# Optimization experiments

Hardware: AMD Instinct MI355X
Metric: run time of the kernel (lower is better)

Reference implementation:

```python
import jax, jax.numpy as jnp
import numpy as np

B, S, E, H = 4, 1024, 1024, 16
HD = E // H  # 64


def setup_inputs() -> dict:
    key = jax.random.key(0)
    ks = jax.random.split(key, 9)
    scale = 1.0 / np.sqrt(E)
    x = jax.random.normal(ks[0], (B, S, E), dtype=jnp.float32)
    attention_mask = jnp.ones((B, S, S), dtype=jnp.int32)
    # per-head projection weights, batched over heads: [H, E, HD]
    Wq = jax.random.normal(ks[1], (H, E, HD), dtype=jnp.float32) * scale
    Wk = jax.random.normal(ks[2], (H, E, HD), dtype=jnp.float32) * scale
    Wv = jax.random.normal(ks[3], (H, E, HD), dtype=jnp.float32) * scale
    bq = jax.random.normal(ks[4], (H, HD), dtype=jnp.float32) * scale
    bk = jax.random.normal(ks[5], (H, HD), dtype=jnp.float32) * scale
    bv = jax.random.normal(ks[6], (H, HD), dtype=jnp.float32) * scale
    # output projection, torch Linear convention: [out_features, in_features]
    Wo = jax.random.normal(ks[7], (E, E), dtype=jnp.float32) * scale
    bo = jax.random.normal(ks[8], (E,), dtype=jnp.float32) * scale
    return {"x": x, "attention_mask": attention_mask, "Wq": Wq, "bq": bq,
            "Wk": Wk, "bk": bk, "Wv": Wv, "bv": bv, "Wo": Wo, "bo": bo}


def reference(x, attention_mask, Wq, bq, Wk, bk, Wv, bv, Wo, bo):
    # batched-over-heads QKV projections: (B,S,E) x (H,E,HD) -> (B,H,S,HD)
    q = jnp.einsum('bse,hed->bhsd', x, Wq) + bq[None, :, None, :]
    k = jnp.einsum('bse,hed->bhsd', x, Wk) + bk[None, :, None, :]
    v = jnp.einsum('bse,hed->bhsd', x, Wv) + bv[None, :, None, :]
    scores = jnp.einsum('bhsd,bhtd->bhst', q, k) / jnp.sqrt(jnp.float32(HD))
    mask = attention_mask[:, None, :, :]  # (B,1,S,S) broadcast over heads
    scores = jnp.where(mask == 0, -jnp.inf, scores)
    weights = jax.nn.softmax(scores, axis=-1)
    out = jnp.einsum('bhst,bhtd->bhsd', weights, v)
    # concat heads on last dim: (B,S,H*HD) == (B,S,E)
    out = out.transpose(0, 2, 1, 3).reshape(B, S, E)
    return out @ Wo.T + bo
```

## Files before the change

### kernel.cpp

```cpp
#include <hip/hip_runtime.h>
#include <hip/hip_bf16.h>

#define NB 4
#define SEQ 1024
#define EMB 1024
#define NH 16
#define HD 64

typedef unsigned short u16;
typedef __attribute__((ext_vector_type(8))) __bf16 bf16x8;
typedef __attribute__((ext_vector_type(8))) short short8;
typedef __attribute__((ext_vector_type(4))) float floatx4;

__device__ inline u16 f2b_rn(float f) {
    union { float f; unsigned int i; } x; x.f = f;
    unsigned int r = (x.i + 0x7FFFu + ((x.i >> 16) & 1u)) >> 16;
    return (u16)r;
}
__device__ inline bf16x8 s2b(short8 v) {
    union { short8 s; bf16x8 b; } x; x.s = v; return x.b;
}

__device__ inline void gload_lds16(const void* g, void* l) {
    __builtin_amdgcn_global_load_lds(
        (const __attribute__((address_space(1))) void*)g,
        (__attribute__((address_space(3))) void*)l, 16, 0, 0);
}

__device__ inline bf16x8 ldsfrag(const u16* base, int r, int c) {
    return s2b(*(const short8*)&base[r * 64 + (c ^ ((r & 7) * 8))]);
}

__device__ inline void cvt8(const float* __restrict__ s, u16* __restrict__ d) {
    float4 a = *(const float4*)(s);
    float4 b = *(const float4*)(s + 4);
    union { u16 u[8]; int4 v; } o;
    o.u[0] = f2b_rn(a.x); o.u[1] = f2b_rn(a.y); o.u[2] = f2b_rn(a.z); o.u[3] = f2b_rn(a.w);
    o.u[4] = f2b_rn(b.x); o.u[5] = f2b_rn(b.y); o.u[6] = f2b_rn(b.z); o.u[7] = f2b_rn(b.w);
    *(int4*)(d) = o.v;
}

__global__ __launch_bounds__(256) void prep(
    const float* __restrict__ x, const float* __restrict__ Wq,
    const float* __restrict__ Wk, const float* __restrict__ Wv,
    u16* __restrict__ xb, u16* __restrict__ Wt)
{
    __shared__ u16 T[64 * 80];
    int bx = blockIdx.x;
    int tid = threadIdx.x;

    if (bx < 512) {
        #pragma unroll
        for (int c = 0; c < 4; ++c) {
            int i = (bx * 4 + c) * 2048 + tid * 8;
            cvt8(x + i, xb + i);
        }
    } else {
        int bx2 = bx - 512;
        int e0 = (bx2 & 15) * 64;
        int ph = bx2 >> 4;
        int p = ph >> 4, h = ph & 15;
        const float* W = (p == 0 ? Wq : (p == 1 ? Wk : Wv)) + h * (EMB * HD);
        #pragma unroll
        for (int c = 0; c < 2; ++c) {
            int flat = c * 2048 + tid * 8;
            int r = flat >> 6;
            int d = flat & 63;
            cvt8(W + (size_t)(e0 + r) * HD + d, &T[r * 80 + d]);
        }
        __syncthreads();
        int d = tid >> 2;
        int ec = tid & 3;
        union { u16 u[16]; int4 v[2]; } tmp;
        #pragma unroll
        for (int i = 0; i < 16; ++i) tmp.u[i] = T[(ec * 16 + i) * 80 + d];
        u16* dst = Wt + ((size_t)(p * NH + h) * HD + d) * EMB + e0 + ec * 16;
        *(int4*)(dst) = tmp.v[0];
        *(int4*)(dst + 8) = tmp.v[1];
    }
}

__global__ __launch_bounds__(256) void qkv_gemm(
    const u16* __restrict__ x,
    const u16* __restrict__ Wt2,
    const float* __restrict__ bq, const float* __restrict__ bk, const float* __restrict__ bv,
    const float* __restrict__ Wo, const int* __restrict__ mask,
    u16* __restrict__ Q, u16* __restrict__ K, u16* __restrict__ Vt,
    u16* __restrict__ Wob, unsigned long long* __restrict__ bits)
{
    __shared__ u16 As[128 * 64];
    __shared__ u16 Bs[128 * 64];

    int gid = blockIdx.x;
    int tid = threadIdx.x;

    if (gid >= 768) {
        if (gid < 1280) {
            int i = (gid - 768) * 2048 + tid * 8;
            cvt8(Wo + i, Wob + i);
        } else {
            int base = (gid - 1280) * 16 + (tid >> 6) * 4;
            int lane = tid & 63;
            #pragma unroll
            for (int i = 0; i < 4; ++i) {
                int gw = base + i;
                int m = mask[(size_t)gw * 64 + lane];
                unsigned long long bl = __ballot(m != 0);
                if (lane == 0) bits[gw] = bl;
            }
        }
        return;
    }

    int n0 = (gid % 24) * 128;
    int m0 = (gid / 24) * 128;
    int w = tid >> 6, lane = tid & 63, quad = lane >> 4, ln = lane & 15;
    int wm = w & 1, wn = w >> 1;

    floatx4 acc[4][4] = {};

    for (int k0 = 0; k0 < EMB; k0 += 64) {
        __syncthreads();
        #pragma unroll
        for (int i = 0; i < 4; ++i) {
            int flat0 = i * 256 + (tid & 192);
            int flat = flat0 + lane;
            int r = flat >> 3;
            int c = ((flat & 7) ^ (r & 7)) * 8;
            gload_lds16(x   + (size_t)(m0 + r) * EMB + k0 + c, As + flat0 * 8);
            gload_lds16(Wt2 + (size_t)(n0 + r) * EMB + k0 + c, Bs + flat0 * 8);
        }
        __syncthreads();

        #pragma unroll
        for (int kk = 0; kk < 2; ++kk) {
            bf16x8 a[4], bf[4];
            #pragma unroll
            for (int mt = 0; mt < 4; ++mt)
                a[mt] = ldsfrag(As, wm * 64 + mt * 16 + ln, kk * 32 + quad * 8);
            #pragma unroll
            for (int nc = 0; nc < 4; ++nc)
                bf[nc] = ldsfrag(Bs, wn * 64 + nc * 16 + ln, kk * 32 + quad * 8);
            #pragma unroll
            for (int mt = 0; mt < 4; ++mt)
                #pragma unroll
                for (int nc = 0; nc < 4; ++nc)
                    acc[mt][nc] = __builtin_amdgcn_mfma_f32_16x16x32_bf16(a[mt], bf[nc], acc[mt][nc], 0, 0, 0);
        }
    }

    int p = n0 >> 10;
    const float* bias = (p == 0 ? bq : (p == 1 ? bk : bv));
    if (p < 2) {
        u16* Out = (p == 0) ? Q : K;
        float qs = (p == 0) ? 0.125f * 1.44269504f : 1.0f;
        #pragma unroll
        for (int nc = 0; nc < 4; ++nc) {
            int n = n0 + wn * 64 + nc * 16 + ln;
            int h = (n >> 6) & 15, d = n & 63;
            float bv_ = bias[n & 1023];
            #pragma unroll
            for (int mt = 0; mt < 4; ++mt) {
                #pragma unroll
                for (int reg = 0; reg < 4; ++reg) {
                    int m = m0 + wm * 64 + mt * 16 + quad * 4 + reg;
                    int b_ = m >> 10, s = m & 1023;
                    Out[((size_t)(b_ * NH + h) * SEQ + s) * HD + d] = f2b_rn((acc[mt][nc][reg] + bv_) * qs);
                }
            }
        }
    } else {
        #pragma unroll
        for (int nc = 0; nc < 4; ++nc) {
            int n = n0 + wn * 64 + nc * 16 + ln;
            int h = (n >> 6) & 15, d = n & 63;
            float bv_ = bias[n & 1023];
            #pragma unroll
            for (int mt = 0; mt < 4; ++mt) {
                int m = m0 + wm * 64 + mt * 16 + quad * 4;
                int b_ = m >> 10, s = m & 1023;
                union { u16 u[4]; uint2 v; } pk;
                #pragma unroll
                for (int reg = 0; reg < 4; ++reg)
                    pk.u[reg] = f2b_rn(acc[mt][nc][reg] + bv_);
                *(uint2*)&Vt[((size_t)(b_ * NH + h) * HD + d) * SEQ + s] = pk.v;
            }
        }
    }
}

__global__ __launch_bounds__(128) void attn(
    const u16* __restrict__ Q, const u16* __restrict__ K, const u16* __restrict__ Vt,
    const unsigned long long* __restrict__ bits,
    u16* __restrict__ Aout)
{
    const int PP = 72;
    __shared__ u16 Ks[64 * 64];
    __shared__ u16 Vs[80 * 64];
    __shared__ u16 Ps[64 * PP];

    int bh = blockIdx.x;
    int q0 = blockIdx.y * 64;
    int b = bh >> 4, h = bh & 15;
    const u16* Qb = Q  + (size_t)bh * SEQ * HD;
    const u16* Kb = K  + (size_t)bh * SEQ * HD;
    const u16* Vb = Vt + (size_t)bh * HD * SEQ;

    int tid = threadIdx.x;
    int w = tid >> 6, lane = tid & 63, quad = lane >> 4, ln = lane & 15;

    if (tid < 16) *(uint2*)&Vs[64 * 64 + tid * 4] = make_uint2(0x3F803F80u, 0x3F803F80u);

    bf16x8 qf[2][2];
    #pragma unroll
    for (int s = 0; s < 2; ++s) {
        const u16* qp = Qb + (size_t)(q0 + w * 32 + s * 16 + ln) * HD + quad * 8;
        union { int4 i; bf16x8 b; } c0, c1;
        c0.i = *(const int4*)(qp);
        c1.i = *(const int4*)(qp + 32);
        qf[s][0] = c0.b; qf[s][1] = c1.b;
    }

    floatx4 o[2][5] = {};

    for (int tt = 0; tt < SEQ / 64; ++tt) {
        int t0 = tt * 64;
        __syncthreads();
        #pragma unroll
        for (int i = 0; i < 4; ++i) {
            int flat0 = i * 128 + (tid & 64);
            int flat = flat0 + lane;
            int r = flat >> 3;
            int c = ((flat & 7) ^ (r & 7)) * 8;
            gload_lds16(Kb + (size_t)(t0 + r) * HD + c, Ks + flat0 * 8);
            gload_lds16(Vb + (size_t)r * SEQ + t0 + c, Vs + flat0 * 8);
        }
        __syncthreads();

        floatx4 sc[2][4] = {};
        #pragma unroll
        for (int kk = 0; kk < 2; ++kk) {
            bf16x8 kf[4];
            #pragma unroll
            for (int tb = 0; tb < 4; ++tb)
                kf[tb] = ldsfrag(Ks, tb * 16 + ln, kk * 32 + quad * 8);
            #pragma unroll
            for (int s = 0; s < 2; ++s)
                #pragma unroll
                for (int tb = 0; tb < 4; ++tb)
                    sc[s][tb] = __builtin_amdgcn_mfma_f32_16x16x32_bf16(kf[tb], qf[s][kk], sc[s][tb], 0, 0, 0);
        }

        #pragma unroll
        for (int s = 0; s < 2; ++s) {
            unsigned long long bm = bits[((size_t)b * SEQ + q0 + w * 32 + s * 16 + ln) * 16 + tt];
            if (__any(bm != ~0ull)) {
                #pragma unroll
                for (int tb = 0; tb < 4; ++tb)
                    #pragma unroll
                    for (int reg = 0; reg < 4; ++reg)
                        if (!((bm >> (tb * 16 + quad * 4 + reg)) & 1)) sc[s][tb][reg] = -1e30f;
            }
        }

        #pragma unroll
        for (int s = 0; s < 2; ++s) {
            int mrow = w * 32 + s * 16 + ln;
            #pragma unroll
            for (int tb = 0; tb < 4; ++tb) {
                union { float f; unsigned int i; } e0_, e1_, e2_, e3_;
                e0_.f = __builtin_amdgcn_exp2f(sc[s][tb][0]);
                e1_.f = __builtin_amdgcn_exp2f(sc[s][tb][1]);
                e2_.f = __builtin_amdgcn_exp2f(sc[s][tb][2]);
                e3_.f = __builtin_amdgcn_exp2f(sc[s][tb][3]);
                uint2 pk;
                pk.x = ((e0_.i + 0x8000u) >> 16) | ((e1_.i + 0x8000u) & 0xFFFF0000u);
                pk.y = ((e2_.i + 0x8000u) >> 16) | ((e3_.i + 0x8000u) & 0xFFFF0000u);
                *(uint2*)&Ps[mrow * PP + tb * 16 + quad * 4] = pk;
            }
        }

        #pragma unroll
        for (int kk = 0; kk < 2; ++kk) {
            bf16x8 vf[5];
            #pragma unroll
            for (int dt = 0; dt < 5; ++dt)
                vf[dt] = ldsfrag(Vs, dt * 16 + ln, kk * 32 + quad * 8);
            #pragma unroll
            for (int s = 0; s < 2; ++s) {
                bf16x8 pf = s2b(*(const short8*)&Ps[(w * 32 + s * 16 + ln) * PP + kk * 32 + quad * 8]);
                #pragma unroll
                for (int dt = 0; dt < 5; ++dt)
                    o[s][dt] = __builtin_amdgcn_mfma_f32_16x16x32_bf16(pf, vf[dt], o[s][dt], 0, 0, 0);
            }
        }
    }

    #pragma unroll
    for (int s = 0; s < 2; ++s) {
        #pragma unroll
        for (int reg = 0; reg < 4; ++reg) {
            float l = __shfl(o[s][4][reg], lane & 48, 64);
            float inv = 1.0f / l;
            int m = q0 + w * 32 + s * 16 + quad * 4 + reg;
            #pragma unroll
            for (int dt = 0; dt < 4; ++dt)
                Aout[((size_t)b * SEQ + m) * EMB + h * HD + dt * 16 + ln] = f2b_rn(o[s][dt][reg] * inv);
        }
    }
}

__global__ __launch_bounds__(256) void out_proj(
    const u16* __restrict__ A,
    const u16* __restrict__ Wo,
    const float* __restrict__ bo,
    float* __restrict__ Out)
{
    __shared__ u16 As[64 * 64];
    __shared__ u16 Bs[128 * 64];

    int m0 = blockIdx.x * 64;
    int n0 = blockIdx.y * 128;
    int tid = threadIdx.x;
    int w = tid >> 6, lane = tid & 63, quad = lane >> 4, ln = lane & 15;
    int wm = w & 1, wn = w >> 1;

    floatx4 acc[2][4] = {};

    for (int k0 = 0; k0 < EMB; k0 += 64) {
        __syncthreads();
        #pragma unroll
        for (int i = 0; i < 2; ++i) {
            int flat0 = i * 256 + (tid & 192);
            int flat = flat0 + lane;
            int r = flat >> 3;
            int c = ((flat & 7) ^ (r & 7)) * 8;
            gload_lds16(A + (size_t)(m0 + r) * EMB + k0 + c, As + flat0 * 8);
        }
        #pragma unroll
        for (int i = 0; i < 4; ++i) {
            int flat0 = i * 256 + (tid & 192);
            int flat = flat0 + lane;
            int r = flat >> 3;
            int c = ((flat & 7) ^ (r & 7)) * 8;
            gload_lds16(Wo + (size_t)(n0 + r) * EMB + k0 + c, Bs + flat0 * 8);
        }
        __syncthreads();

        #pragma unroll
        for (int kk = 0; kk < 2; ++kk) {
            bf16x8 a[2], bfr[4];
            #pragma unroll
            for (int mt = 0; mt < 2; ++mt)
                a[mt] = ldsfrag(As, wm * 32 + mt * 16 + ln, kk * 32 + quad * 8);
            #pragma unroll
            for (int nc = 0; nc < 4; ++nc)
                bfr[nc] = ldsfrag(Bs, wn * 64 + nc * 16 + ln, kk * 32 + quad * 8);
            #pragma unroll
            for (int mt = 0; mt < 2; ++mt)
                #pragma unroll
                for (int nc = 0; nc < 4; ++nc)
                    acc[mt][nc] = __builtin_amdgcn_mfma_f32_16x16x32_bf16(a[mt], bfr[nc], acc[mt][nc], 0, 0, 0);
        }
    }

    #pragma unroll
    for (int nc = 0; nc < 4; ++nc) {
        int n = n0 + wn * 64 + nc * 16 + ln;
        float bb = bo[n];
        #pragma unroll
        for (int mt = 0; mt < 2; ++mt) {
            #pragma unroll
            for (int reg = 0; reg < 4; ++reg) {
                int m = m0 + wm * 32 + mt * 16 + quad * 4 + reg;
                Out[(size_t)m * EMB + n] = acc[mt][nc][reg] + bb;
            }
        }
    }
}

extern "C" void kernel_launch(void* const* d_in, const int* in_sizes, int n_in,
                              void* d_out, int out_size, void* d_ws, size_t ws_size,
                              hipStream_t stream) {
    const float* x  = (const float*)d_in[0];
    const int*   mk = (const int*)d_in[1];
    const float* Wq = (const float*)d_in[2];
    const float* bq = (const float*)d_in[3];
    const float* Wk = (const float*)d_in[4];
    const float* bk = (const float*)d_in[5];
    const float* Wv = (const float*)d_in[6];
    const float* bv = (const float*)d_in[7];
    const float* Wo = (const float*)d_in[8];
    const float* bo = (const float*)d_in[9];
    float* out = (float*)d_out;

    const size_t MB = 1u << 20;
    char* ws = (char*)d_ws;
    u16* xb  = (u16*)ws;
    u16* Wt  = (u16*)(ws + 8 * MB);
    u16* Wob = (u16*)(ws + 14 * MB);
    unsigned long long* bits = (unsigned long long*)(ws + 16 * MB);
    u16* Qw  = (u16*)(ws + 16 * MB + 512 * 1024);
    u16* Kw  = (u16*)(ws + 24 * MB + 512 * 1024);
    u16* Vtw = (u16*)(ws + 32 * MB + 512 * 1024);
    u16* Ao  = xb;

    prep<<<1280, 256, 0, stream>>>(x, Wq, Wk, Wv, xb, Wt);
    qkv_gemm<<<5376, 256, 0, stream>>>(
        xb, Wt, bq, bk, bv, Wo, mk, Qw, Kw, Vtw, Wob, bits);
    attn<<<dim3(NB * NH, SEQ / 64), 128, 0, stream>>>(Qw, Kw, Vtw, bits, Ao);
    out_proj<<<dim3((NB * SEQ) / 64, EMB / 128), 256, 0, stream>>>(Ao, Wob, bo, out);
}
```

Baseline: 198.0 us.

## Fuse all four stages into one persistent kernel with grid-wide barriers

Replaces the separate prep, QKV GEMM, attention and output-projection launches with a single persistent kernel of 768 blocks. The stages are separated by atomic-counter grid barriers, and the counter is reset by a memset before each launch. Shared memory is a union sized for the largest stage, and attention blocks now use 256 threads covering 128 query rows. The goal is to remove launch gaps and tail effects between kernels. In exchange it adds spin-wait barriers, leaves a third of the blocks idle in the later stages, and depends on all blocks being co-resident.

```diff
diff --git a/kernel.cpp b/kernel.cpp
--- a/kernel.cpp
+++ b/kernel.cpp
@@ -6,6 +6,7 @@
 #define EMB 1024
 #define NH 16
 #define HD 64
+#define GRID 768
 
 typedef unsigned short u16;
 typedef __attribute__((ext_vector_type(8))) __bf16 bf16x8;
@@ -20,17 +21,14 @@
 __device__ inline bf16x8 s2b(short8 v) {
     union { short8 s; bf16x8 b; } x; x.s = v; return x.b;
 }
-
 __device__ inline void gload_lds16(const void* g, void* l) {
     __builtin_amdgcn_global_load_lds(
         (const __attribute__((address_space(1))) void*)g,
         (__attribute__((address_space(3))) void*)l, 16, 0, 0);
 }
-
 __device__ inline bf16x8 ldsfrag(const u16* base, int r, int c) {
     return s2b(*(const short8*)&base[r * 64 + (c ^ ((r & 7) * 8))]);
 }
-
 __device__ inline void cvt8(const float* __restrict__ s, u16* __restrict__ d) {
     float4 a = *(const float4*)(s);
     float4 b = *(const float4*)(s + 4);
@@ -40,25 +38,45 @@
     *(int4*)(d) = o.v;
 }
 
-__global__ __launch_bounds__(256) void prep(
-    const float* __restrict__ x, const float* __restrict__ Wq,
-    const float* __restrict__ Wk, const float* __restrict__ Wv,
-    u16* __restrict__ xb, u16* __restrict__ Wt)
+__device__ inline void grid_sync(unsigned int* cnt, unsigned int target) {
+    __syncthreads();
+    if (threadIdx.x == 0) {
+        __threadfence();
+        atomicAdd(cnt, 1u);
+        while (atomicAdd(cnt, 0u) < target) __builtin_amdgcn_s_sleep(8);
+        __threadfence();
+    }
+    __syncthreads();
+}
+
+union SharedU {
+    u16 T[64 * 80];
+    struct { u16 As[128 * 64]; u16 Bs[128 * 64]; } g;
+    struct { u16 Ks[64 * 64]; u16 Vs[80 * 64]; u16 Ps[128 * 72]; } a;
+    struct { u16 As[64 * 64]; u16 Bs[128 * 64]; } p;
+};
+
+__global__ __launch_bounds__(256, 3) void fused_mha(
+    const float* __restrict__ x, const int* __restrict__ mask,
+    const float* __restrict__ Wq, const float* __restrict__ Wk, const float* __restrict__ Wv,
+    const float* __restrict__ Wo,
+    const float* __restrict__ bq, const float* __restrict__ bk, const float* __restrict__ bv,
+    const float* __restrict__ bo,
+    u16* __restrict__ xb, u16* __restrict__ Wt, u16* __restrict__ Wob,
+    unsigned long long* __restrict__ bits,
+    u16* __restrict__ Q, u16* __restrict__ K, u16* __restrict__ Vt,
+    u16* __restrict__ Ao, float* __restrict__ Out,
+    unsigned int* __restrict__ cnt)
 {
-    __shared__ u16 T[64 * 80];
-    int bx = blockIdx.x;
+    __shared__ SharedU lds;
+    int bid = blockIdx.x;
     int tid = threadIdx.x;
-
-    if (bx < 512) {
-        #pragma unroll
-        for (int c = 0; c < 4; ++c) {
-            int i = (bx * 4 + c) * 2048 + tid * 8;
-            cvt8(x + i, xb + i);
-        }
-    } else {
-        int bx2 = bx - 512;
-        int e0 = (bx2 & 15) * 64;
-        int ph = bx2 >> 4;
+    int lane = tid & 63, quad = lane >> 4, ln = lane & 15;
+    int w = tid >> 6;
+
+    {
+        int e0 = (bid & 15) * 64;
+        int ph = bid >> 4;
         int p = ph >> 4, h = ph & 15;
         const float* W = (p == 0 ? Wq : (p == 1 ? Wk : Wv)) + h * (EMB * HD);
         #pragma unroll
@@ -66,41 +84,29 @@
             int flat = c * 2048 + tid * 8;
             int r = flat >> 6;
             int d = flat & 63;
-            cvt8(W + (size_t)(e0 + r) * HD + d, &T[r * 80 + d]);
+            cvt8(W + (size_t)(e0 + r) * HD + d, &lds.T[r * 80 + d]);
         }
         __syncthreads();
         int d = tid >> 2;
         int ec = tid & 3;
         union { u16 u[16]; int4 v[2]; } tmp;
         #pragma unroll
-        for (int i = 0; i < 16; ++i) tmp.u[i] = T[(ec * 16 + i) * 80 + d];
+        for (int i = 0; i < 16; ++i) tmp.u[i] = lds.T[(ec * 16 + i) * 80 + d];
         u16* dst = Wt + ((size_t)(p * NH + h) * HD + d) * EMB + e0 + ec * 16;
         *(int4*)(dst) = tmp.v[0];
         *(int4*)(dst + 8) = tmp.v[1];
-    }
-}
-
-__global__ __launch_bounds__(256) void qkv_gemm(
-    const u16* __restrict__ x,
-    const u16* __restrict__ Wt2,
-    const float* __restrict__ bq, const float* __restrict__ bk, const float* __restrict__ bv,
-    const float* __restrict__ Wo, const int* __restrict__ mask,
-    u16* __restrict__ Q, u16* __restrict__ K, u16* __restrict__ Vt,
-    u16* __restrict__ Wob, unsigned long long* __restrict__ bits)
-{
-    __shared__ u16 As[128 * 64];
-    __shared__ u16 Bs[128 * 64];
-
-    int gid = blockIdx.x;
-    int tid = threadIdx.x;
-
-    if (gid >= 768) {
-        if (gid < 1280) {
-            int i = (gid - 768) * 2048 + tid * 8;
+
+        if (bid < 512) {
+            #pragma unroll
+            for (int c = 0; c < 4; ++c) {
+                int i = (bid * 4 + c) * 2048 + tid * 8;
+                cvt8(x + i, xb + i);
+            }
+            int i = bid * 2048 + tid * 8;
             cvt8(Wo + i, Wob + i);
-        } else {
-            int base = (gid - 1280) * 16 + (tid >> 6) * 4;
-            int lane = tid & 63;
+        }
+        for (int u = bid; u < 4096; u += GRID) {
+            int base = u * 16 + w * 4;
             #pragma unroll
             for (int i = 0; i < 4; ++i) {
                 int gw = base + i;
@@ -109,271 +115,261 @@
                 if (lane == 0) bits[gw] = bl;
             }
         }
-        return;
     }
-
-    int n0 = (gid % 24) * 128;
-    int m0 = (gid / 24) * 128;
-    int w = tid >> 6, lane = tid & 63, quad = lane >> 4, ln = lane & 15;
-    int wm = w & 1, wn = w >> 1;
-
-    floatx4 acc[4][4] = {};
-
-    for (int k0 = 0; k0 < EMB; k0 += 64) {
-        __syncthreads();
+    grid_sync(cnt, GRID);
+
+    {
+        u16* As = lds.g.As;
+        u16* Bs = lds.g.Bs;
+        int n0 = (bid % 24) * 128;
+        int m0 = (bid / 24) * 128;
+        int wm = w & 1, wn = w >> 1;
+
+        floatx4 acc[4][4] = {};
+
+        for (int k0 = 0; k0 < EMB; k0 += 64) {
+            __syncthreads();
+            #pragma unroll
+            for (int i = 0; i < 4; ++i) {
+                int flat0 = i * 256 + (tid & 192);
+                int flat = flat0 + lane;
+                int r = flat >> 3;
+                int c = ((flat & 7) ^ (r & 7)) * 8;
+                gload_lds16(xb + (size_t)(m0 + r) * EMB + k0 + c, As + flat0 * 8);
+                gload_lds16(Wt + (size_t)(n0 + r) * EMB + k0 + c, Bs + flat0 * 8);
+            }
+            __syncthreads();
+
+            #pragma unroll
+            for (int kk = 0; kk < 2; ++kk) {
+                bf16x8 a[4], bf[4];
+                #pragma unroll
+                for (int mt = 0; mt < 4; ++mt)
+                    a[mt] = ldsfrag(As, wm * 64 + mt * 16 + ln, kk * 32 + quad * 8);
+                #pragma unroll
+                for (int nc = 0; nc < 4; ++nc)
+                    bf[nc] = ldsfrag(Bs, wn * 64 + nc * 16 + ln, kk * 32 + quad * 8);
+                #pragma unroll
+                for (int mt = 0; mt < 4; ++mt)
+                    #pragma unroll
+                    for (int nc = 0; nc < 4; ++nc)
+                        acc[mt][nc] = __builtin_amdgcn_mfma_f32_16x16x32_bf16(a[mt], bf[nc], acc[mt][nc], 0, 0, 0);
+            }
+        }
+
+        int p = n0 >> 10;
+        const float* bias = (p == 0 ? bq : (p == 1 ? bk : bv));
+        if (p < 2) {
+            u16* Outp = (p == 0) ? Q : K;
+            float qs = (p == 0) ? 0.125f * 1.44269504f : 1.0f;
+            #pragma unroll
+            for (int nc = 0; nc < 4; ++nc) {
+                int n = n0 + wn * 64 + nc * 16 + ln;
+                int h = (n >> 6) & 15, d = n & 63;
+                float bv_ = bias[n & 1023];
+                #pragma unroll
+                for (int mt = 0; mt < 4; ++mt) {
+                    #pragma unroll
+                    for (int reg = 0; reg < 4; ++reg) {
+                        int m = m0 + wm * 64 + mt * 16 + quad * 4 + reg;
+                        int b_ = m >> 10, s = m & 1023;
+                        Outp[((size_t)(b_ * NH + h) * SEQ + s) * HD + d] = f2b_rn((acc[mt][nc][reg] + bv_) * qs);
+                    }
+                }
+            }
+        } else {
+            #pragma unroll
+            for (int nc = 0; nc < 4; ++nc) {
+                int n = n0 + wn * 64 + nc * 16 + ln;
+                int h = (n >> 6) & 15, d = n & 63;
+                float bv_ = bias[n & 1023];
+                #pragma unroll
+                for (int mt = 0; mt < 4; ++mt) {
+                    int m = m0 + wm * 64 + mt * 16 + quad * 4;
+                    int b_ = m >> 10, s = m & 1023;
+                    union { u16 u[4]; uint2 v; } pk;
+                    #pragma unroll
+                    for (int reg = 0; reg < 4; ++reg)
+                        pk.u[reg] = f2b_rn(acc[mt][nc][reg] + bv_);
+                    *(uint2*)&Vt[((size_t)(b_ * NH + h) * HD + d) * SEQ + s] = pk.v;
+                }
+            }
+        }
+    }
+    grid_sync(cnt, 2 * GRID);
+
+    if (bid < 512) {
+        u16* Ks = lds.a.Ks;
+        u16* Vs = lds.a.Vs;
+        u16* Ps = lds.a.Ps;
+        const int PP = 72;
+
+        int bh = bid & 63;
+        int q0 = (bid >> 6) * 128;
+        int b = bh >> 4, h = bh & 15;
+        const u16* Qb = Q  + (size_t)bh * SEQ * HD;
+        const u16* Kb = K  + (size_t)bh * SEQ * HD;
+        const u16* Vb = Vt + (size_t)bh * HD * SEQ;
+
+        if (tid < 16) *(uint2*)&Vs[64 * 64 + tid * 4] = make_uint2(0x3F803F80u, 0x3F803F80u);
+
+        bf16x8 qf[2][2];
         #pragma unroll
-        for (int i = 0; i < 4; ++i) {
-            int flat0 = i * 256 + (tid & 192);
-            int flat = flat0 + lane;
-            int r = flat >> 3;
-            int c = ((flat & 7) ^ (r & 7)) * 8;
-            gload_lds16(x   + (size_t)(m0 + r) * EMB + k0 + c, As + flat0 * 8);
-            gload_lds16(Wt2 + (size_t)(n0 + r) * EMB + k0 + c, Bs + flat0 * 8);
-        }
-        __syncthreads();
+        for (int s = 0; s < 2; ++s) {
+            const u16* qp = Qb + (size_t)(q0 + w * 32 + s * 16 + ln) * HD + quad * 8;
+            union { int4 i; bf16x8 b; } c0, c1;
+            c0.i = *(const int4*)(qp);
+            c1.i = *(const int4*)(qp + 32);
+            qf[s][0] = c0.b; qf[s][1] = c1.b;
+        }
+
+        floatx4 o[2][5] = {};
+
+        for (int tt = 0; tt < SEQ / 64; ++tt) {
+            int t0 = tt * 64;
+            __syncthreads();
+            #pragma unroll
+            for (int i = 0; i < 2; ++i) {
+                int flat0 = i * 256 + (tid & 192);
+                int flat = flat0 + lane;
+                int r = flat >> 3;
+                int c = ((flat & 7) ^ (r & 7)) * 8;
+                gload_lds16(Kb + (size_t)(t0 + r) * HD + c, Ks + flat0 * 8);
+                gload_lds16(Vb + (size_t)r * SEQ + t0 + c, Vs + flat0 * 8);
+            }
+            __syncthreads();
+
+            floatx4 sc[2][4] = {};
+            #pragma unroll
+            for (int kk = 0; kk < 2; ++kk) {
+                bf16x8 kf[4];
+                #pragma unroll
+                for (int tb = 0; tb < 4; ++tb)
+                    kf[tb] = ldsfrag(Ks, tb * 16 + ln, kk * 32 + quad * 8);
+                #pragma unroll
+                for (int s = 0; s < 2; ++s)
+                    #pragma unroll
+                    for (int tb = 0; tb < 4; ++tb)
+                        sc[s][tb] = __builtin_amdgcn_mfma_f32_16x16x32_bf16(kf[tb], qf[s][kk], sc[s][tb], 0, 0, 0);
+            }
+
+            #pragma unroll
+            for (int s = 0; s < 2; ++s) {
+                unsigned long long bm = bits[((size_t)b * SEQ + q0 + w * 32 + s * 16 + ln) * 16 + tt];
+                if (__any(bm != ~0ull)) {
+                    #pragma unroll
+                    for (int tb = 0; tb < 4; ++tb)
+                        #pragma unroll
+                        for (int reg = 0; reg < 4; ++reg)
+                            if (!((bm >> (tb * 16 + quad * 4 + reg)) & 1)) sc[s][tb][reg] = -1e30f;
+                }
+            }
+
+            #pragma unroll
+            for (int s = 0; s < 2; ++s) {
+                int mrow = w * 32 + s * 16 + ln;
+                #pragma unroll
+                for (int tb = 0; tb < 4; ++tb) {
+                    union { float f; unsigned int i; } e0_, e1_, e2_, e3_;
+                    e0_.f = __builtin_amdgcn_exp2f(sc[s][tb][0]);
+                    e1_.f = __builtin_amdgcn_exp2f(sc[s][tb][1]);
+                    e2_.f = __builtin_amdgcn_exp2f(sc[s][tb][2]);
+                    e3_.f = __builtin_amdgcn_exp2f(sc[s][tb][3]);
+                    uint2 pk;
+                    pk.x = ((e0_.i + 0x8000u) >> 16) | ((e1_.i + 0x8000u) & 0xFFFF0000u);
+                    pk.y = ((e2_.i + 0x8000u) >> 16) | ((e3_.i + 0x8000u) & 0xFFFF0000u);
+                    *(uint2*)&Ps[mrow * PP + tb * 16 + quad * 4] = pk;
+                }
+            }
+
+            #pragma unroll
+            for (int kk = 0; kk < 2; ++kk) {
+                bf16x8 vf[5];
+                #pragma unroll
+                for (int dt = 0; dt < 5; ++dt)
+                    vf[dt] = ldsfrag(Vs, dt * 16 + ln, kk * 32 + quad * 8);
+                #pragma unroll
+                for (int s = 0; s < 2; ++s) {
+                    bf16x8 pf = s2b(*(const short8*)&Ps[(w * 32 + s * 16 + ln) * PP + kk * 32 + quad * 8]);
+                    #pragma unroll
+                    for (int dt = 0; dt < 5; ++dt)
+                        o[s][dt] = __builtin_amdgcn_mfma_f32_16x16x32_bf16(pf, vf[dt], o[s][dt], 0, 0, 0);
+                }
+            }
+        }
 
         #pragma unroll
-        for (int kk = 0; kk < 2; ++kk) {
-            bf16x8 a[4], bf[4];
-            #pragma unroll
-            for (int mt = 0; mt < 4; ++mt)
-                a[mt] = ldsfrag(As, wm * 64 + mt * 16 + ln, kk * 32 + quad * 8);
-            #pragma unroll
-            for (int nc = 0; nc < 4; ++nc)
-                bf[nc] = ldsfrag(Bs, wn * 64 + nc * 16 + ln, kk * 32 + quad * 8);
-            #pragma unroll
-            for (int mt = 0; mt < 4; ++mt)
+        for (int s = 0; s < 2; ++s) {
+            #pragma unroll
+            for (int reg = 0; reg < 4; ++reg) {
+                float l = __shfl(o[s][4][reg], lane & 48, 64);
+                float inv = 1.0f / l;
+                int m = q0 + w * 32 + s * 16 + quad * 4 + reg;
+                #pragma unroll
+                for (int dt = 0; dt < 4; ++dt)
+                    Ao[((size_t)b * SEQ + m) * EMB + h * HD + dt * 16 + ln] = f2b_rn(o[s][dt][reg] * inv);
+            }
+        }
+    }
+    grid_sync(cnt, 3 * GRID);
+
+    if (bid < 512) {
+        u16* As = lds.p.As;
+        u16* Bs = lds.p.Bs;
+        int m0 = (bid & 63) * 64;
+        int n0 = (bid >> 6) * 128;
+        int wm = w & 1, wn = w >> 1;
+
+        floatx4 acc[2][4] = {};
+
+        for (int k0 = 0; k0 < EMB; k0 += 64) {
+            __syncthreads();
+            #pragma unroll
+            for (int i = 0; i < 2; ++i) {
+                int flat0 = i * 256 + (tid & 192);
+                int flat = flat0 + lane;
+                int r = flat >> 3;
+                int c = ((flat & 7) ^ (r & 7)) * 8;
+                gload_lds16(Ao + (size_t)(m0 + r) * EMB + k0 + c, As + flat0 * 8);
+            }
+            #pragma unroll
+            for (int i = 0; i < 4; ++i) {
+                int flat0 = i * 256 + (tid & 192);
+                int flat = flat0 + lane;
+                int r = flat >> 3;
+                int c = ((flat & 7) ^ (r & 7)) * 8;
+                gload_lds16(Wob + (size_t)(n0 + r) * EMB + k0 + c, Bs + flat0 * 8);
+            }
+            __syncthreads();
+
+            #pragma unroll
+            for (int kk = 0; kk < 2; ++kk) {
+                bf16x8 a[2], bfr[4];
+                #pragma unroll
+                for (int mt = 0; mt < 2; ++mt)
+                    a[mt] = ldsfrag(As, wm * 32 + mt * 16 + ln, kk * 32 + quad * 8);
                 #pragma unroll
                 for (int nc = 0; nc < 4; ++nc)
-                    acc[mt][nc] = __builtin_amdgcn_mfma_f32_16x16x32_bf16(a[mt], bf[nc], acc[mt][nc], 0, 0, 0);
-        }
-    }
-
-    int p = n0 >> 10;
-    const float* bias = (p == 0 ? bq : (p == 1 ? bk : bv));
-    if (p < 2) {
-        u16* Out = (p == 0) ? Q : K;
-        float qs = (p == 0) ? 0.125f * 1.44269504f : 1.0f;
+                    bfr[nc] = ldsfrag(Bs, wn * 64 + nc * 16 + ln, kk * 32 + quad * 8);
+                #pragma unroll
+                for (int mt = 0; mt < 2; ++mt)
+                    #pragma unroll
+                    for (int nc = 0; nc < 4; ++nc)
+                        acc[mt][nc] = __builtin_amdgcn_mfma_f32_16x16x32_bf16(a[mt], bfr[nc], acc[mt][nc], 0, 0, 0);
+            }
+        }
+
         #pragma unroll
         for (int nc = 0; nc < 4; ++nc) {
             int n = n0 + wn * 64 + nc * 16 + ln;
-            int h = (n >> 6) & 15, d = n & 63;
-            float bv_ = bias[n & 1023];
-            #pragma unroll
-            for (int mt = 0; mt < 4; ++mt) {
+            float bb = bo[n];
+            #pragma unroll
+            for (int mt = 0; mt < 2; ++mt) {
                 #pragma unroll
                 for (int reg = 0; reg < 4; ++reg) {
-                    int m = m0 + wm * 64 + mt * 16 + quad * 4 + reg;
-                    int b_ = m >> 10, s = m & 1023;
-                    Out[((size_t)(b_ * NH + h) * SEQ + s) * HD + d] = f2b_rn((acc[mt][nc][reg] + bv_) * qs);
-                }
-            }
-        }
-    } else {
-        #pragma unroll
-        for (int nc = 0; nc < 4; ++nc) {
-            int n = n0 + wn * 64 + nc * 16 + ln;
-            int h = (n >> 6) & 15, d = n & 63;
-            float bv_ = bias[n & 1023];
-            #pragma unroll
-            for (int mt = 0; mt < 4; ++mt) {
-                int m = m0 + wm * 64 + mt * 16 + quad * 4;
-                int b_ = m >> 10, s = m & 1023;
-                union { u16 u[4]; uint2 v; } pk;
-                #pragma unroll
-                for (int reg = 0; reg < 4; ++reg)
-                    pk.u[reg] = f2b_rn(acc[mt][nc][reg] + bv_);
-                *(uint2*)&Vt[((size_t)(b_ * NH + h) * HD + d) * SEQ + s] = pk.v;
-            }
-        }
-    }
-}
-
-__global__ __launch_bounds__(128) void attn(
-    const u16* __restrict__ Q, const u16* __restrict__ K, const u16* __restrict__ Vt,
-    const unsigned long long* __restrict__ bits,
-    u16* __restrict__ Aout)
-{
-    const int PP = 72;
-    __shared__ u16 Ks[64 * 64];
-    __shared__ u16 Vs[80 * 64];
-    __shared__ u16 Ps[64 * PP];
-
-    int bh = blockIdx.x;
-    int q0 = blockIdx.y * 64;
-    int b = bh >> 4, h = bh & 15;
-    const u16* Qb = Q  + (size_t)bh * SEQ * HD;
-    const u16* Kb = K  + (size_t)bh * SEQ * HD;
-    const u16* Vb = Vt + (size_t)bh * HD * SEQ;
-
-    int tid = threadIdx.x;
-    int w = tid >> 6, lane = tid & 63, quad = lane >> 4, ln = lane & 15;
-
-    if (tid < 16) *(uint2*)&Vs[64 * 64 + tid * 4] = make_uint2(0x3F803F80u, 0x3F803F80u);
-
-    bf16x8 qf[2][2];
-    #pragma unroll
-    for (int s = 0; s < 2; ++s) {
-        const u16* qp = Qb + (size_t)(q0 + w * 32 + s * 16 + ln) * HD + quad * 8;
-        union { int4 i; bf16x8 b; } c0, c1;
-        c0.i = *(const int4*)(qp);
-        c1.i = *(const int4*)(qp + 32);
-        qf[s][0] = c0.b; qf[s][1] = c1.b;
-    }
-
-    floatx4 o[2][5] = {};
-
-    for (int tt = 0; tt < SEQ / 64; ++tt) {
-        int t0 = tt * 64;
-        __syncthreads();
-        #pragma unroll
-        for (int i = 0; i < 4; ++i) {
-            int flat0 = i * 128 + (tid & 64);
-            int flat = flat0 + lane;
-            int r = flat >> 3;
-            int c = ((flat & 7) ^ (r & 7)) * 8;
-            gload_lds16(Kb + (size_t)(t0 + r) * HD + c, Ks + flat0 * 8);
-            gload_lds16(Vb + (size_t)r * SEQ + t0 + c, Vs + flat0 * 8);
-        }
-        __syncthreads();
-
-        floatx4 sc[2][4] = {};
-        #pragma unroll
-        for (int kk = 0; kk < 2; ++kk) {
-            bf16x8 kf[4];
-            #pragma unroll
-            for (int tb = 0; tb < 4; ++tb)
-                kf[tb] = ldsfrag(Ks, tb * 16 + ln, kk * 32 + quad * 8);
-            #pragma unroll
-            for (int s = 0; s < 2; ++s)
-                #pragma unroll
-                for (int tb = 0; tb < 4; ++tb)
-                    sc[s][tb] = __builtin_amdgcn_mfma_f32_16x16x32_bf16(kf[tb], qf[s][kk], sc[s][tb], 0, 0, 0);
-        }
-
-        #pragma unroll
-        for (int s = 0; s < 2; ++s) {
-            unsigned long long bm = bits[((size_t)b * SEQ + q0 + w * 32 + s * 16 + ln) * 16 + tt];
-            if (__any(bm != ~0ull)) {
-                #pragma unroll
-                for (int tb = 0; tb < 4; ++tb)
-                    #pragma unroll
-                    for (int reg = 0; reg < 4; ++reg)
-                        if (!((bm >> (tb * 16 + quad * 4 + reg)) & 1)) sc[s][tb][reg] = -1e30f;
-            }
-        }
-
-        #pragma unroll
-        for (int s = 0; s < 2; ++s) {
-            int mrow = w * 32 + s * 16 + ln;
-            #pragma unroll
-            for (int tb = 0; tb < 4; ++tb) {
-                union { float f; unsigned int i; } e0_, e1_, e2_, e3_;
-                e0_.f = __builtin_amdgcn_exp2f(sc[s][tb][0]);
-                e1_.f = __builtin_amdgcn_exp2f(sc[s][tb][1]);
-                e2_.f = __builtin_amdgcn_exp2f(sc[s][tb][2]);
-                e3_.f = __builtin_amdgcn_exp2f(sc[s][tb][3]);
-                uint2 pk;
-                pk.x = ((e0_.i + 0x8000u) >> 16) | ((e1_.i + 0x8000u) & 0xFFFF0000u);
-                pk.y = ((e2_.i + 0x8000u) >> 16) | ((e3_.i + 0x8000u) & 0xFFFF0000u);
-                *(uint2*)&Ps[mrow * PP + tb * 16 + quad * 4] = pk;
-            }
-        }
-
-        #pragma unroll
-        for (int kk = 0; kk < 2; ++kk) {
-            bf16x8 vf[5];
-            #pragma unroll
-            for (int dt = 0; dt < 5; ++dt)
-                vf[dt] = ldsfrag(Vs, dt * 16 + ln, kk * 32 + quad * 8);
-            #pragma unroll
-            for (int s = 0; s < 2; ++s) {
-                bf16x8 pf = s2b(*(const short8*)&Ps[(w * 32 + s * 16 + ln) * PP + kk * 32 + quad * 8]);
-                #pragma unroll
-                for (int dt = 0; dt < 5; ++dt)
-                    o[s][dt] = __builtin_amdgcn_mfma_f32_16x16x32_bf16(pf, vf[dt], o[s][dt], 0, 0, 0);
-            }
-        }
-    }
-
-    #pragma unroll
-    for (int s = 0; s < 2; ++s) {
-        #pragma unroll
-        for (int reg = 0; reg < 4; ++reg) {
-            float l = __shfl(o[s][4][reg], lane & 48, 64);
-            float inv = 1.0f / l;
-            int m = q0 + w * 32 + s * 16 + quad * 4 + reg;
-            #pragma unroll
-            for (int dt = 0; dt < 4; ++dt)
-                Aout[((size_t)b * SEQ + m) * EMB + h * HD + dt * 16 + ln] = f2b_rn(o[s][dt][reg] * inv);
-        }
-    }
-}
-
-__global__ __launch_bounds__(256) void out_proj(
-    const u16* __restrict__ A,
-    const u16* __restrict__ Wo,
-    const float* __restrict__ bo,
-    float* __restrict__ Out)
-{
-    __shared__ u16 As[64 * 64];
-    __shared__ u16 Bs[128 * 64];
-
-    int m0 = blockIdx.x * 64;
-    int n0 = blockIdx.y * 128;
-    int tid = threadIdx.x;
-    int w = tid >> 6, lane = tid & 63, quad = lane >> 4, ln = lane & 15;
-    int wm = w & 1, wn = w >> 1;
-
-    floatx4 acc[2][4] = {};
-
-    for (int k0 = 0; k0 < EMB; k0 += 64) {
-        __syncthreads();
-        #pragma unroll
-        for (int i = 0; i < 2; ++i) {
-            int flat0 = i * 256 + (tid & 192);
-            int flat = flat0 + lane;
-            int r = flat >> 3;
-            int c = ((flat & 7) ^ (r & 7)) * 8;
-            gload_lds16(A + (size_t)(m0 + r) * EMB + k0 + c, As + flat0 * 8);
-        }
-        #pragma unroll
-        for (int i = 0; i < 4; ++i) {
-            int flat0 = i * 256 + (tid & 192);
-            int flat = flat0 + lane;
-            int r = flat >> 3;
-            int c = ((flat & 7) ^ (r & 7)) * 8;
-            gload_lds16(Wo + (size_t)(n0 + r) * EMB + k0 + c, Bs + flat0 * 8);
-        }
-        __syncthreads();
-
-        #pragma unroll
-        for (int kk = 0; kk < 2; ++kk) {
-            bf16x8 a[2], bfr[4];
-            #pragma unroll
-            for (int mt = 0; mt < 2; ++mt)
-                a[mt] = ldsfrag(As, wm * 32 + mt * 16 + ln, kk * 32 + quad * 8);
-            #pragma unroll
-            for (int nc = 0; nc < 4; ++nc)
-                bfr[nc] = ldsfrag(Bs, wn * 64 + nc * 16 + ln, kk * 32 + quad * 8);
-            #pragma unroll
-            for (int mt = 0; mt < 2; ++mt)
-                #pragma unroll
-                for (int nc = 0; nc < 4; ++nc)
-                    acc[mt][nc] = __builtin_amdgcn_mfma_f32_16x16x32_bf16(a[mt], bfr[nc], acc[mt][nc], 0, 0, 0);
-        }
-    }
-
-    #pragma unroll
-    for (int nc = 0; nc < 4; ++nc) {
-        int n = n0 + wn * 64 + nc * 16 + ln;
-        float bb = bo[n];
-        #pragma unroll
-        for (int mt = 0; mt < 2; ++mt) {
-            #pragma unroll
-            for (int reg = 0; reg < 4; ++reg) {
-                int m = m0 + wm * 32 + mt * 16 + quad * 4 + reg;
-                Out[(size_t)m * EMB + n] = acc[mt][nc][reg] + bb;
+                    int m = m0 + wm * 32 + mt * 16 + quad * 4 + reg;
+                    Out[(size_t)m * EMB + n] = acc[mt][nc][reg] + bb;
+                }
             }
         }
     }
@@ -403,11 +399,11 @@
     u16* Qw  = (u16*)(ws + 16 * MB + 512 * 1024);
     u16* Kw  = (u16*)(ws + 24 * MB + 512 * 1024);
     u16* Vtw = (u16*)(ws + 32 * MB + 512 * 1024);
+    unsigned int* cnt = (unsigned int*)(ws + 41 * MB);
     u16* Ao  = xb;
 
-    prep<<<1280, 256, 0, stream>>>(x, Wq, Wk, Wv, xb, Wt);
-    qkv_gemm<<<5376, 256, 0, stream>>>(
-        xb, Wt, bq, bk, bv, Wo, mk, Qw, Kw, Vtw, Wob, bits);
-    attn<<<dim3(NB * NH, SEQ / 64), 128, 0, stream>>>(Qw, Kw, Vtw, bits, Ao);
-    out_proj<<<dim3((NB * SEQ) / 64, EMB / 128), 256, 0, stream>>>(Ao, Wob, bo, out);
-}
+    hipMemsetAsync(cnt, 0, 4, stream);
+    fused_mha<<<GRID, 256, 0, stream>>>(
+        x, mk, Wq, Wk, Wv, Wo, bq, bk, bv, bo,
+        xb, Wt, Wob, bits, Qw, Kw, Vtw, Ao, out, cnt);
+}
```

After: 486.3 us. 146% more time.

## Redistribute side tasks: mask bit-packing into prep, Wo conversion into attention

Applied to the files above, without the earlier changes.

Moves the mask-to-bitmask ballot work out of the QKV GEMM launch and into the prep kernel. It also moves the Wo fp32-to-bf16 conversion into extra blocks of the attention kernel, which now uses a flattened 1D grid. The GEMM launch then holds only its 768 compute blocks, with no branch or extra register pressure from tail blocks. Light elementwise work now overlaps with the heavier attention and prep kernels. Extra tail blocks in attention could change scheduling, and each Wo block now converts half as much data.

```diff
diff --git a/kernel.cpp b/kernel.cpp
--- a/kernel.cpp
+++ b/kernel.cpp
@@ -43,7 +43,9 @@
 __global__ __launch_bounds__(256) void prep(
     const float* __restrict__ x, const float* __restrict__ Wq,
     const float* __restrict__ Wk, const float* __restrict__ Wv,
-    u16* __restrict__ xb, u16* __restrict__ Wt)
+    const int* __restrict__ mask,
+    u16* __restrict__ xb, u16* __restrict__ Wt,
+    unsigned long long* __restrict__ bits)
 {
     __shared__ u16 T[64 * 80];
     int bx = blockIdx.x;
@@ -55,7 +57,7 @@
             int i = (bx * 4 + c) * 2048 + tid * 8;
             cvt8(x + i, xb + i);
         }
-    } else {
+    } else if (bx < 1280) {
         int bx2 = bx - 512;
         int e0 = (bx2 & 15) * 64;
         int ph = bx2 >> 4;
@@ -77,6 +79,16 @@
         u16* dst = Wt + ((size_t)(p * NH + h) * HD + d) * EMB + e0 + ec * 16;
         *(int4*)(dst) = tmp.v[0];
         *(int4*)(dst + 8) = tmp.v[1];
+    } else {
+        int base = (bx - 1280) * 16 + (tid >> 6) * 4;
+        int lane = tid & 63;
+        #pragma unroll
+        for (int i = 0; i < 4; ++i) {
+            int gw = base + i;
+            int m = mask[(size_t)gw * 64 + lane];
+            unsigned long long bl = __ballot(m != 0);
+            if (lane == 0) bits[gw] = bl;
+        }
     }
 }
 
@@ -84,36 +96,15 @@
     const u16* __restrict__ x,
     const u16* __restrict__ Wt2,
     const float* __restrict__ bq, const float* __restrict__ bk, const float* __restrict__ bv,
-    const float* __restrict__ Wo, const int* __restrict__ mask,
-    u16* __restrict__ Q, u16* __restrict__ K, u16* __restrict__ Vt,
-    u16* __restrict__ Wob, unsigned long long* __restrict__ bits)
+    u16* __restrict__ Q, u16* __restrict__ K, u16* __restrict__ Vt)
 {
     __shared__ u16 As[128 * 64];
     __shared__ u16 Bs[128 * 64];
 
     int gid = blockIdx.x;
-    int tid = threadIdx.x;
-
-    if (gid >= 768) {
-        if (gid < 1280) {
-            int i = (gid - 768) * 2048 + tid * 8;
-            cvt8(Wo + i, Wob + i);
-        } else {
-            int base = (gid - 1280) * 16 + (tid >> 6) * 4;
-            int lane = tid & 63;
-            #pragma unroll
-            for (int i = 0; i < 4; ++i) {
-                int gw = base + i;
-                int m = mask[(size_t)gw * 64 + lane];
-                unsigned long long bl = __ballot(m != 0);
-                if (lane == 0) bits[gw] = bl;
-            }
-        }
-        return;
-    }
-
     int n0 = (gid % 24) * 128;
     int m0 = (gid / 24) * 128;
+    int tid = threadIdx.x;
     int w = tid >> 6, lane = tid & 63, quad = lane >> 4, ln = lane & 15;
     int wm = w & 1, wn = w >> 1;
 
@@ -192,6 +183,7 @@
 __global__ __launch_bounds__(128) void attn(
     const u16* __restrict__ Q, const u16* __restrict__ K, const u16* __restrict__ Vt,
     const unsigned long long* __restrict__ bits,
+    const float* __restrict__ Wo, u16* __restrict__ Wob,
     u16* __restrict__ Aout)
 {
     const int PP = 72;
@@ -199,14 +191,22 @@
     __shared__ u16 Vs[80 * 64];
     __shared__ u16 Ps[64 * PP];
 
-    int bh = blockIdx.x;
-    int q0 = blockIdx.y * 64;
+    int bid = blockIdx.x;
+    int tid = threadIdx.x;
+
+    if (bid >= 1024) {
+        int i = (bid - 1024) * 1024 + tid * 8;
+        cvt8(Wo + i, Wob + i);
+        return;
+    }
+
+    int bh = bid & 63;
+    int q0 = (bid >> 6) * 64;
     int b = bh >> 4, h = bh & 15;
     const u16* Qb = Q  + (size_t)bh * SEQ * HD;
     const u16* Kb = K  + (size_t)bh * SEQ * HD;
     const u16* Vb = Vt + (size_t)bh * HD * SEQ;
 
-    int tid = threadIdx.x;
     int w = tid >> 6, lane = tid & 63, quad = lane >> 4, ln = lane & 15;
 
     if (tid < 16) *(uint2*)&Vs[64 * 64 + tid * 4] = make_uint2(0x3F803F80u, 0x3F803F80u);
@@ -405,9 +405,8 @@
     u16* Vtw = (u16*)(ws + 32 * MB + 512 * 1024);
     u16* Ao  = xb;
 
-    prep<<<1280, 256, 0, stream>>>(x, Wq, Wk, Wv, xb, Wt);
-    qkv_gemm<<<5376, 256, 0, stream>>>(
-        xb, Wt, bq, bk, bv, Wo, mk, Qw, Kw, Vtw, Wob, bits);
-    attn<<<dim3(NB * NH, SEQ / 64), 128, 0, stream>>>(Qw, Kw, Vtw, bits, Ao);
+    prep<<<5376, 256, 0, stream>>>(x, Wq, Wk, Wv, mk, xb, Wt, bits);
+    qkv_gemm<<<768, 256, 0, stream>>>(xb, Wt, bq, bk, bv, Qw, Kw, Vtw);
+    attn<<<2048, 128, 0, stream>>>(Qw, Kw, Vtw, bits, Wo, Wob, Ao);
     out_proj<<<dim3((NB * SEQ) / 64, EMB / 128), 256, 0, stream>>>(Ao, Wob, bo, out);
 }
```

Result: no change. 198.7 us (+0.3%).
